# Kernel optimization log

Hardware: AMD Instinct MI355X
Metric: run time of the kernel (lower is better)

## Reference

```python
import jax, jax.numpy as jnp
import numpy as np

B, L, V, H = 4096, 80, 256, 512  # batch, NLE_TERM_CO, charset, msg_hdim


def setup_inputs() -> dict:
    key = jax.random.key(0)
    k0, k1, k2 = jax.random.split(key, 3)
    message = jax.random.randint(k0, (B, L), 0, V, dtype=jnp.int64)
    # Linear(i_dim=L*V, H): store weight as [L*V, H] (i.e. torch weight.T)
    W1 = jax.random.normal(k1, (L * V, H), dtype=jnp.float32) * 0.01
    b1 = jnp.zeros((H,), dtype=jnp.float32)
    W2 = jax.random.normal(k2, (H, H), dtype=jnp.float32) * 0.02
    b2 = jnp.zeros((H,), dtype=jnp.float32)
    return {"message": message, "W1": W1, "b1": b1, "W2": W2, "b2": b2}


def reference(message, W1, b1, W2, b2):
    # one_hot(message, 256).reshape(B, L*256) @ W1  ==  gather rows of W1 at
    # flat index pos*256 + char, summed over positions (no one-hot materialized).
    idx = message + jnp.arange(L, dtype=message.dtype)[None, :] * V  # [B, L]
    emb = jnp.take(W1, idx, axis=0).sum(axis=1)                       # [B, H]
    h = jax.nn.relu(emb + b1)
    out = jax.nn.relu(h @ W2 + b2)
    return out
```

## Files before the change

kernel.cpp:

```cpp
#include <hip/hip_runtime.h>
#include <hip/hip_bf16.h>
#include <stdint.h>

#define B_ 4096
#define L_ 80
#define V_ 256
#define H_ 512

typedef __attribute__((ext_vector_type(4))) float f32x4;
typedef __attribute__((ext_vector_type(8))) short bf16x8;

__global__ __launch_bounds__(256) void w2_transpose(
    const float* __restrict__ W2, __hip_bfloat16* __restrict__ W2T) {
  int i = blockIdx.x * blockDim.x + threadIdx.x;
  int n = i >> 9, k = i & 511;
  W2T[i] = __float2bfloat16(W2[k * H_ + n]);
}

__global__ __launch_bounds__(512) void encode_gather(
    const int* __restrict__ msg, const float* __restrict__ W1,
    const float* __restrict__ b1, __hip_bfloat16* __restrict__ h) {
  const int BT = 16;
  __shared__ int offs[BT * L_];
  const int t = threadIdx.x;
  const int b0 = blockIdx.x * BT;

  for (int i = t; i < BT * L_; i += 512) {
    int b = i / L_, l = i - b * L_;
    offs[i] = (l * V_ + msg[(b0 + b) * L_ + l]) * H_;
  }
  __syncthreads();

  float acc[BT];
#pragma unroll
  for (int b = 0; b < BT; ++b) acc[b] = 0.f;

  for (int l = 0; l < L_; ++l) {
#pragma unroll
    for (int b = 0; b < BT; ++b) {
      acc[b] += W1[offs[b * L_ + l] + t];
    }
  }

  const float bias = b1[t];
#pragma unroll
  for (int b = 0; b < BT; ++b) {
    float v = acc[b] + bias;
    v = v > 0.f ? v : 0.f;
    h[(size_t)(b0 + b) * H_ + t] = __float2bfloat16(v);
  }
}

__global__ __launch_bounds__(256) void gemm_out(
    const __hip_bfloat16* __restrict__ h, const __hip_bfloat16* __restrict__ W2T,
    const float* __restrict__ b2, float* __restrict__ out) {
  const int wid = threadIdx.x >> 6;
  const int lane = threadIdx.x & 63;
  const int wm = wid >> 1, wn = wid & 1;
  const int bm = blockIdx.x * 64;
  const int bn = blockIdx.y * 64;
  const int lr = lane & 15;
  const int lq = lane >> 4;

  f32x4 acc[2][2] = {};

  const __hip_bfloat16* aptr0 = h + (size_t)(bm + wm * 32 + lr) * H_ + lq * 8;
  const __hip_bfloat16* bptr0 = W2T + (size_t)(bn + wn * 32 + lr) * H_ + lq * 8;

  for (int kt = 0; kt < H_ / 32; ++kt) {
    const int ko = kt * 32;
    bf16x8 a[2], bfr[2];
#pragma unroll
    for (int mi = 0; mi < 2; ++mi)
      a[mi] = *reinterpret_cast<const bf16x8*>(aptr0 + (size_t)mi * 16 * H_ + ko);
#pragma unroll
    for (int ni = 0; ni < 2; ++ni)
      bfr[ni] = *reinterpret_cast<const bf16x8*>(bptr0 + (size_t)ni * 16 * H_ + ko);
#pragma unroll
    for (int mi = 0; mi < 2; ++mi)
#pragma unroll
      for (int ni = 0; ni < 2; ++ni)
        acc[mi][ni] = __builtin_amdgcn_mfma_f32_16x16x32_bf16(
            a[mi], bfr[ni], acc[mi][ni], 0, 0, 0);
  }

#pragma unroll
  for (int mi = 0; mi < 2; ++mi) {
#pragma unroll
    for (int ni = 0; ni < 2; ++ni) {
      const int n = bn + wn * 32 + ni * 16 + lr;
      const float bias = b2[n];
#pragma unroll
      for (int r = 0; r < 4; ++r) {
        const int m = bm + wm * 32 + mi * 16 + lq * 4 + r;
        float v = acc[mi][ni][r] + bias;
        out[(size_t)m * H_ + n] = v > 0.f ? v : 0.f;
      }
    }
  }
}

extern "C" void kernel_launch(void* const* d_in, const int* in_sizes, int n_in,
                              void* d_out, int out_size, void* d_ws, size_t ws_size,
                              hipStream_t stream) {
  const int* msg   = (const int*)d_in[0];
  const float* W1  = (const float*)d_in[1];
  const float* b1  = (const float*)d_in[2];
  const float* W2  = (const float*)d_in[3];
  const float* b2  = (const float*)d_in[4];
  float* out = (float*)d_out;

  __hip_bfloat16* W2T = (__hip_bfloat16*)d_ws;
  __hip_bfloat16* h   = (__hip_bfloat16*)((char*)d_ws + H_ * H_ * 2);

  hipLaunchKernelGGL(w2_transpose, dim3((H_ * H_) / 256), dim3(256), 0, stream,
                     W2, W2T);
  hipLaunchKernelGGL(encode_gather, dim3(B_ / 16), dim3(512), 0, stream,
                     msg, W1, b1, h);
  hipLaunchKernelGGL(gemm_out, dim3(B_ / 64, H_ / 64), dim3(256), 0, stream,
                     h, W2T, b2, out);
}
```

Baseline: 149.8 us.

## Vectorize gather, tile W2 transpose via LDS, enlarge GEMM M tile

The W2 transpose now goes through a padded shared-memory tile, so both its reads and writes are coalesced. The gather kernel uses 8 rows per block, with each thread loading float4 chunks of W1 at wave-uniform offsets (readfirstlane) and storing packed bf16x4. The GEMM block tile doubles in M to 128, giving each wave 4x2 MFMA tiles for more operand reuse. A manual round-to-nearest-even bf16 conversion replaces the library call, and it does not handle NaN specially.

Result: slower. 165.9 us (+10.7%).

```diff
diff --git a/kernel.cpp b/kernel.cpp
--- a/kernel.cpp
+++ b/kernel.cpp
@@ -10,20 +10,38 @@
 typedef __attribute__((ext_vector_type(4))) float f32x4;
 typedef __attribute__((ext_vector_type(8))) short bf16x8;
 
+static __device__ __forceinline__ unsigned short f2bf(float x) {
+  union { float f; unsigned int u; } a;
+  a.f = x;
+  unsigned int r = a.u + 0x7fffu + ((a.u >> 16) & 1u);
+  return (unsigned short)(r >> 16);
+}
+
 __global__ __launch_bounds__(256) void w2_transpose(
-    const float* __restrict__ W2, __hip_bfloat16* __restrict__ W2T) {
-  int i = blockIdx.x * blockDim.x + threadIdx.x;
-  int n = i >> 9, k = i & 511;
-  W2T[i] = __float2bfloat16(W2[k * H_ + n]);
+    const float* __restrict__ W2, unsigned short* __restrict__ W2T) {
+  __shared__ float tile[32][33];
+  const int ti = blockIdx.x;
+  const int tj = blockIdx.y;
+  const int r = threadIdx.x >> 5;
+  const int c = threadIdx.x & 31;
+#pragma unroll
+  for (int rr = r; rr < 32; rr += 8)
+    tile[rr][c] = W2[(size_t)(ti * 32 + rr) * H_ + tj * 32 + c];
+  __syncthreads();
+#pragma unroll
+  for (int rr = r; rr < 32; rr += 8)
+    W2T[(size_t)(tj * 32 + rr) * H_ + ti * 32 + c] = f2bf(tile[c][rr]);
 }
 
 __global__ __launch_bounds__(512) void encode_gather(
     const int* __restrict__ msg, const float* __restrict__ W1,
-    const float* __restrict__ b1, __hip_bfloat16* __restrict__ h) {
-  const int BT = 16;
+    const float* __restrict__ b1, unsigned short* __restrict__ h) {
+  const int BT = 8;
   __shared__ int offs[BT * L_];
   const int t = threadIdx.x;
   const int b0 = blockIdx.x * BT;
+  const int g = t >> 7;
+  const int c4 = (t & 127) * 4;
 
   for (int i = t; i < BT * L_; i += 512) {
     int b = i / L_, l = i - b * L_;
@@ -31,68 +49,74 @@
   }
   __syncthreads();
 
-  float acc[BT];
-#pragma unroll
-  for (int b = 0; b < BT; ++b) acc[b] = 0.f;
+  const int br0 = g * 2, br1 = g * 2 + 1;
+  f32x4 acc0 = {}, acc1 = {};
 
+#pragma unroll 4
   for (int l = 0; l < L_; ++l) {
-#pragma unroll
-    for (int b = 0; b < BT; ++b) {
-      acc[b] += W1[offs[b * L_ + l] + t];
-    }
+    int o0 = __builtin_amdgcn_readfirstlane(offs[br0 * L_ + l]);
+    int o1 = __builtin_amdgcn_readfirstlane(offs[br1 * L_ + l]);
+    acc0 += *reinterpret_cast<const f32x4*>(W1 + o0 + c4);
+    acc1 += *reinterpret_cast<const f32x4*>(W1 + o1 + c4);
   }
 
-  const float bias = b1[t];
-#pragma unroll
-  for (int b = 0; b < BT; ++b) {
-    float v = acc[b] + bias;
-    v = v > 0.f ? v : 0.f;
-    h[(size_t)(b0 + b) * H_ + t] = __float2bfloat16(v);
-  }
+  const f32x4 bias = *reinterpret_cast<const f32x4*>(b1 + c4);
+  f32x4 v0 = acc0 + bias, v1 = acc1 + bias;
+  ushort4 o0, o1;
+  o0.x = f2bf(v0[0] > 0.f ? v0[0] : 0.f);
+  o0.y = f2bf(v0[1] > 0.f ? v0[1] : 0.f);
+  o0.z = f2bf(v0[2] > 0.f ? v0[2] : 0.f);
+  o0.w = f2bf(v0[3] > 0.f ? v0[3] : 0.f);
+  o1.x = f2bf(v1[0] > 0.f ? v1[0] : 0.f);
+  o1.y = f2bf(v1[1] > 0.f ? v1[1] : 0.f);
+  o1.z = f2bf(v1[2] > 0.f ? v1[2] : 0.f);
+  o1.w = f2bf(v1[3] > 0.f ? v1[3] : 0.f);
+  *reinterpret_cast<ushort4*>(&h[(size_t)(b0 + br0) * H_ + c4]) = o0;
+  *reinterpret_cast<ushort4*>(&h[(size_t)(b0 + br1) * H_ + c4]) = o1;
 }
 
 __global__ __launch_bounds__(256) void gemm_out(
-    const __hip_bfloat16* __restrict__ h, const __hip_bfloat16* __restrict__ W2T,
+    const unsigned short* __restrict__ h, const unsigned short* __restrict__ W2T,
     const float* __restrict__ b2, float* __restrict__ out) {
   const int wid = threadIdx.x >> 6;
   const int lane = threadIdx.x & 63;
   const int wm = wid >> 1, wn = wid & 1;
-  const int bm = blockIdx.x * 64;
+  const int bm = blockIdx.x * 128;
   const int bn = blockIdx.y * 64;
   const int lr = lane & 15;
   const int lq = lane >> 4;
 
-  f32x4 acc[2][2] = {};
+  f32x4 acc[4][2] = {};
 
-  const __hip_bfloat16* aptr0 = h + (size_t)(bm + wm * 32 + lr) * H_ + lq * 8;
-  const __hip_bfloat16* bptr0 = W2T + (size_t)(bn + wn * 32 + lr) * H_ + lq * 8;
+  const unsigned short* aptr = h + (size_t)(bm + wm * 64 + lr) * H_ + lq * 8;
+  const unsigned short* bptr = W2T + (size_t)(bn + wn * 32 + lr) * H_ + lq * 8;
 
   for (int kt = 0; kt < H_ / 32; ++kt) {
     const int ko = kt * 32;
-    bf16x8 a[2], bfr[2];
+    bf16x8 a[4], bb[2];
 #pragma unroll
-    for (int mi = 0; mi < 2; ++mi)
-      a[mi] = *reinterpret_cast<const bf16x8*>(aptr0 + (size_t)mi * 16 * H_ + ko);
+    for (int mi = 0; mi < 4; ++mi)
+      a[mi] = *reinterpret_cast<const bf16x8*>(aptr + (size_t)mi * 16 * H_ + ko);
 #pragma unroll
     for (int ni = 0; ni < 2; ++ni)
-      bfr[ni] = *reinterpret_cast<const bf16x8*>(bptr0 + (size_t)ni * 16 * H_ + ko);
+      bb[ni] = *reinterpret_cast<const bf16x8*>(bptr + (size_t)ni * 16 * H_ + ko);
 #pragma unroll
-    for (int mi = 0; mi < 2; ++mi)
+    for (int mi = 0; mi < 4; ++mi)
 #pragma unroll
       for (int ni = 0; ni < 2; ++ni)
         acc[mi][ni] = __builtin_amdgcn_mfma_f32_16x16x32_bf16(
-            a[mi], bfr[ni], acc[mi][ni], 0, 0, 0);
+            a[mi], bb[ni], acc[mi][ni], 0, 0, 0);
   }
 
 #pragma unroll
-  for (int mi = 0; mi < 2; ++mi) {
+  for (int mi = 0; mi < 4; ++mi) {
 #pragma unroll
     for (int ni = 0; ni < 2; ++ni) {
       const int n = bn + wn * 32 + ni * 16 + lr;
       const float bias = b2[n];
 #pragma unroll
       for (int r = 0; r < 4; ++r) {
-        const int m = bm + wm * 32 + mi * 16 + lq * 4 + r;
+        const int m = bm + wm * 64 + mi * 16 + lq * 4 + r;
         float v = acc[mi][ni][r] + bias;
         out[(size_t)m * H_ + n] = v > 0.f ? v : 0.f;
       }
@@ -110,13 +134,13 @@
   const float* b2  = (const float*)d_in[4];
   float* out = (float*)d_out;
 
-  __hip_bfloat16* W2T = (__hip_bfloat16*)d_ws;
-  __hip_bfloat16* h   = (__hip_bfloat16*)((char*)d_ws + H_ * H_ * 2);
+  unsigned short* W2T = (unsigned short*)d_ws;
+  unsigned short* h   = (unsigned short*)((char*)d_ws + H_ * H_ * 2);
 
-  hipLaunchKernelGGL(w2_transpose, dim3((H_ * H_) / 256), dim3(256), 0, stream,
+  hipLaunchKernelGGL(w2_transpose, dim3(H_ / 32, H_ / 32), dim3(256), 0, stream,
                      W2, W2T);
-  hipLaunchKernelGGL(encode_gather, dim3(B_ / 16), dim3(512), 0, stream,
+  hipLaunchKernelGGL(encode_gather, dim3(B_ / 8), dim3(512), 0, stream,
                      msg, W1, b1, h);
-  hipLaunchKernelGGL(gemm_out, dim3(B_ / 64, H_ / 64), dim3(256), 0, stream,
+  hipLaunchKernelGGL(gemm_out, dim3(B_ / 128, H_ / 64), dim3(256), 0, stream,
                      h, W2T, b2, out);
 }
```
